# Kernel tuning notes

Measured on AMD Instinct MI355X. Metric: run time of the kernel, lower is better.

Reference implementation:

```python
import jax, jax.numpy as jnp
import numpy as np

R, K, CF, HF, WF = 64, 81, 256, 256, 256  # ROIs, classes(incl bg), FPN channels, P2 size
IMG = 1024.0
SCALE = 0.25          # P2 feature stride 4
STEPS = 4             # subdivision steps: 7 -> 112
NPTS = 28 * 28        # subdivision_num_points
FC = 256


def _grid_sample(img, coords):
    """torch.grid_sample(bilinear, align_corners=False, zeros padding).
    img: [N,C,H,W]; coords: [N,P,2] (x,y) in [0,1]. Returns [N,C,P]."""
    N, C, H, W = img.shape
    x = coords[..., 0] * W - 0.5
    y = coords[..., 1] * H - 0.5
    x0 = jnp.floor(x); y0 = jnp.floor(y)
    fx = x - x0; fy = y - y0

    def g(ix, iy, w):
        valid = (ix >= 0) & (ix < W) & (iy >= 0) & (iy < H)
        ixc = jnp.clip(ix, 0, W - 1).astype(jnp.int32)
        iyc = jnp.clip(iy, 0, H - 1).astype(jnp.int32)
        v = jax.vmap(lambda im, yy, xx: im[:, yy, xx])(img, iyc, ixc)  # [N,C,P]
        return v * (w * valid)[:, None, :]

    return (g(x0, y0, (1 - fx) * (1 - fy)) + g(x0 + 1, y0, fx * (1 - fy))
            + g(x0, y0 + 1, (1 - fx) * fy) + g(x0 + 1, y0 + 1, fx * fy))


def _point_head(fine, coarse, W1, b1, W2, b2, W3, b3, Wp, bp):
    # StandardPointHead: 1x1-conv fc layers, coarse logits re-concatenated each layer
    x = jnp.concatenate([fine, coarse], axis=1)  # [R, CF+K, P]
    for Wl, bl in ((W1, b1), (W2, b2), (W3, b3)):
        x = jax.nn.relu(jnp.einsum('oc,rcp->rop', Wl, x) + bl[None, :, None])
        x = jnp.concatenate([x, coarse], axis=1)
    return jnp.einsum('oc,rcp->rop', Wp, x) + bp[None, :, None]  # [R,K,P]


def setup_inputs() -> dict:
    key = jax.random.key(0)
    ks = jax.random.split(key, 12)
    feat = jax.random.normal(ks[0], (1, CF, HF, WF), dtype=jnp.float32)
    u = jax.random.uniform(ks[1], (R, 4), dtype=jnp.float32)
    x0 = u[:, 0] * (IMG - 256.0); y0 = u[:, 1] * (IMG - 256.0)
    w = 32.0 + u[:, 2] * 224.0;   h = 32.0 + u[:, 3] * 224.0
    det_bboxes = jnp.stack([x0, y0, x0 + w, y0 + h], axis=1)
    det_labels = jax.random.randint(ks[2], (R,), 0, 80, dtype=jnp.int32)
    coarse_logits = jax.random.normal(ks[3], (R, K, 7, 7), dtype=jnp.float32)
    cin = CF + K  # = FC + K = 337 for all layers here
    s = 0.02
    return {
        'feat': feat, 'det_bboxes': det_bboxes, 'det_labels': det_labels,
        'coarse_logits': coarse_logits,
        'W1': jax.random.normal(ks[4], (FC, cin), jnp.float32) * s,
        'b1': jnp.zeros((FC,), jnp.float32),
        'W2': jax.random.normal(ks[5], (FC, FC + K), jnp.float32) * s,
        'b2': jnp.zeros((FC,), jnp.float32),
        'W3': jax.random.normal(ks[6], (FC, FC + K), jnp.float32) * s,
        'b3': jnp.zeros((FC,), jnp.float32),
        'Wp': jax.random.normal(ks[7], (K, FC + K), jnp.float32) * s,
        'bp': jnp.zeros((K,), jnp.float32),
    }


def reference(feat, det_bboxes, det_labels, coarse_logits,
              W1, b1, W2, b2, W3, b3, Wp, bp):
    ml = coarse_logits
    bx0, by0 = det_bboxes[:, 0], det_bboxes[:, 1]
    bw = det_bboxes[:, 2] - det_bboxes[:, 0]
    bh = det_bboxes[:, 3] - det_bboxes[:, 1]
    for step in range(STEPS):
        _, _, H, W = ml.shape
        H, W = 2 * H, 2 * W
        # bilinear x2, align_corners=False (half-pixel centers)
        ml = jax.image.resize(ml, (R, K, H, W), method='linear')
        if NPTS >= 4 * H * W and step < STEPS - 1:
            continue
        # uncertainty = -|logit of gt class| (det_labels+1 skips background ch 0)
        gt = ml[jnp.arange(R), det_labels + 1]              # [R,H,W]
        unc = -jnp.abs(gt).reshape(R, H * W)
        _, idx = jax.lax.top_k(unc, NPTS)                   # [R,NPTS]
        px = ((idx % W).astype(ml.dtype) + 0.5) / W
        py = ((idx // W).astype(ml.dtype) + 0.5) / H
        coords = jnp.stack([px, py], axis=-1)               # [R,NPTS,2] in ROI [0,1]
        # project ROI coords to image, then to P2 normalized coords
        cx = bx0[:, None] + coords[..., 0] * bw[:, None]
        cy = by0[:, None] + coords[..., 1] * bh[:, None]
        fcoords = jnp.stack([cx * SCALE / WF, cy * SCALE / HF], axis=-1)
        fine = _grid_sample(feat, fcoords.reshape(1, R * NPTS, 2))  # [1,CF,R*NPTS]
        fine = fine[0].reshape(CF, R, NPTS).transpose(1, 0, 2)      # [R,CF,NPTS]
        coarse = _grid_sample(coarse_logits, coords)                # [R,K,NPTS]
        pl = _point_head(fine, coarse, W1, b1, W2, b2, W3, b3, Wp, bp)
        ml = jax.vmap(lambda m, i, p: m.at[:, i].set(p))(
            ml.reshape(R, K, H * W), idx, pl).reshape(R, K, H, W)
    return ml
```

## Files before the change

### kernel.cpp

```cpp
#include <hip/hip_runtime.h>
#include <hip/hip_bf16.h>
#include <cstdint>
#include <cstddef>

#define R_ 64
#define K_ 81
#define NPTS_ 784

typedef __attribute__((ext_vector_type(8))) short short8;
typedef __attribute__((ext_vector_type(4))) float f32x4;

#define GLDS16(G, L)                                                           \
  __builtin_amdgcn_global_load_lds(                                            \
      (__attribute__((address_space(1))) void*)(void*)(G),                     \
      (__attribute__((address_space(3))) void*)(L), 16, 0, 0)

__global__ __launch_bounds__(256) void transpose_feat_kernel(const float* __restrict__ in,
                                                             float* __restrict__ out) {
  __shared__ float tile[32][33];
  int y = blockIdx.z;
  int x0 = blockIdx.x * 32, c0 = blockIdx.y * 32;
  int tx = threadIdx.x, ty = threadIdx.y;
#pragma unroll
  for (int j = 0; j < 32; j += 8)
    tile[ty + j][tx] = in[(size_t)(c0 + ty + j) * 65536 + (size_t)y * 256 + x0 + tx];
  __syncthreads();
#pragma unroll
  for (int j = 0; j < 32; j += 8)
    out[((size_t)y * 256 + (x0 + ty + j)) * 256 + c0 + tx] = tile[tx][ty + j];
}

__global__ void transpose_coarse_kernel(const float* __restrict__ in, float* __restrict__ out) {
  int t = blockIdx.x * 256 + threadIdx.x;
  if (t >= R_ * 49 * K_) return;
  int k = t % K_;
  int t2 = t / K_;
  int pos = t2 % 49;
  int r = t2 / 49;
  out[t] = in[((size_t)r * K_ + k) * 49 + pos];
}

__global__ void prep_wpack_kernel(const float* __restrict__ W1, const float* __restrict__ W2,
                                  const float* __restrict__ W3, const float* __restrict__ Wp,
                                  const float* __restrict__ b1, const float* __restrict__ b2,
                                  const float* __restrict__ b3, const float* __restrict__ bp,
                                  __hip_bfloat16* __restrict__ Wpk, float* __restrict__ bias_all) {
  int t = blockIdx.x * 256 + threadIdx.x;
  if (t < 90112) {
    int lane = t & 63;
    int t2 = t >> 6;
    int hl = t2 & 1;
    t2 >>= 1;
    int jg = t2 & 15;
    t2 >>= 4;
    int kt = t2 % 11;
    int L = t2 / 11;
    int o = jg * 16 + (lane & 15);
    int kbase = kt * 32 + (lane >> 4) * 8;
    const float* Wsrc = (L == 0) ? W1 : (L == 1) ? W2 : (L == 2) ? W3 : Wp;
    int Omax = (L == 3) ? 81 : 256;
    __hip_bfloat16 outv[8];
#pragma unroll
    for (int e = 0; e < 8; ++e) {
      int k = kbase + e;
      float v = (o < Omax && k < 337) ? Wsrc[o * 337 + k] : 0.f;
      __hip_bfloat16 h = __float2bfloat16(v);
      outv[e] = hl ? __float2bfloat16(v - __bfloat162float(h)) : h;
    }
    *(short8*)(Wpk + (size_t)t * 8) = *(const short8*)outv;
  } else if (t < 90112 + 1024) {
    int k = t - 90112;
    float v = 0.f;
    if (k < 256) v = b1[k];
    else if (k < 512) v = b2[k - 256];
    else if (k < 768) v = b3[k - 512];
    else if (k < 768 + 81) v = bp[k - 768];
    bias_all[k] = v;
  }
}

__global__ __launch_bounds__(128) void upsample2x_kernel(const float* __restrict__ in,
                                                         float* __restrict__ out,
                                                         int Hin, int Win) {
  int b = blockIdx.z;
  int iy = blockIdx.y * 2 + threadIdx.y;
  int ix = blockIdx.x * 64 + threadIdx.x;
  if (ix >= Win || iy >= Hin) return;
  const float* p = in + (size_t)b * Hin * Win;
  int rT = (iy == 0) ? 0 : iy - 1;
  int rB = (iy == Hin - 1) ? iy : iy + 1;
  int cL = (ix == 0) ? 0 : ix - 1;
  int cR = (ix == Win - 1) ? ix : ix + 1;
  float wyT1 = (iy == 0) ? 0.f : 0.75f;
  float wyB1 = (iy == Hin - 1) ? 0.f : 0.25f;
  float wxE1 = (ix == 0) ? 0.f : 0.75f;
  float wxO1 = (ix == Win - 1) ? 0.f : 0.25f;
  float wyT0 = 1.f - wyT1, wyB0 = 1.f - wyB1;
  float wxE0 = 1.f - wxE1, wxO0 = 1.f - wxO1;

  const float* rowA = p + (size_t)rT * Win;
  const float* rowM = p + (size_t)iy * Win;
  const float* rowC = p + (size_t)rB * Win;
  float al = rowA[cL], am = rowA[ix], ar = rowA[cR];
  float mL = rowM[cL], mm = rowM[ix], mr = rowM[cR];
  float cl = rowC[cL], cm = rowC[ix], cr = rowC[cR];

  float aE = wxE0 * al + wxE1 * am;
  float aO = wxO0 * am + wxO1 * ar;
  float mE = wxE0 * mL + wxE1 * mm;
  float mO = wxO0 * mm + wxO1 * mr;
  float cE = wxE0 * cl + wxE1 * cm;
  float cO = wxO0 * cm + wxO1 * cr;

  float oTE = wyT0 * aE + wyT1 * mE;
  float oTO = wyT0 * aO + wyT1 * mO;
  float oBE = wyB0 * mE + wyB1 * cE;
  float oBO = wyB0 * mO + wyB1 * cO;

  int Wout = 2 * Win;
  float* ob = out + ((size_t)b * (2 * Hin) + 2 * iy) * Wout + 2 * ix;
  *(float2*)ob = make_float2(oTE, oTO);
  *(float2*)(ob + Wout) = make_float2(oBE, oBO);
}

__global__ void iota_kernel(int* __restrict__ sel) {
  int t = blockIdx.x * 256 + threadIdx.x;
  if (t < R_ * NPTS_) sel[t] = t % NPTS_;
}

__global__ __launch_bounds__(256) void topk_kernel(const float* __restrict__ ml,
                                                   const int* __restrict__ labels,
                                                   int N, int* __restrict__ sel) {
  int r = blockIdx.x;
  const float* gt = ml + ((size_t)r * K_ + (labels[r] + 1)) * N;
  __shared__ unsigned int hist[256];
  __shared__ unsigned int sh_prefix, sh_remaining, sh_countless;
  int tid = threadIdx.x;

  unsigned int prefix = 0;
  unsigned int remaining = NPTS_;
  unsigned int count_less = 0;
  for (int pass = 0; pass < 4; ++pass) {
    int shift = 24 - 8 * pass;
    hist[tid] = 0;
    __syncthreads();
    for (int i = tid; i < N; i += 256) {
      unsigned int v = __float_as_uint(fabsf(gt[i]));
      bool match = (pass == 0) || ((v >> (shift + 8)) == prefix);
      if (match) atomicAdd(&hist[(v >> shift) & 255u], 1u);
    }
    __syncthreads();
    if (tid == 0) {
      unsigned int cum = 0, before = 0;
      int d = 255;
      for (int dd = 0; dd < 256; ++dd) {
        unsigned int c = hist[dd];
        if (cum + c >= remaining) { before = cum; d = dd; break; }
        cum += c;
      }
      sh_prefix = (prefix << 8) | (unsigned int)d;
      sh_remaining = remaining - before;
      sh_countless = count_less + before;
    }
    __syncthreads();
    prefix = sh_prefix;
    remaining = sh_remaining;
    count_less = sh_countless;
    __syncthreads();
  }
  unsigned int vstar = prefix;
  unsigned int need_eq = NPTS_ - count_less;

  __shared__ unsigned int wtot_less[4], wtot_eq[4];
  unsigned int base_less = 0, base_eq = 0;
  int lane = tid & 63, wv = tid >> 6;
  int* selr = sel + (size_t)r * NPTS_;
  for (int base = 0; base < N; base += 256) {
    int i = base + tid;
    bool less = false, eq = false;
    if (i < N) {
      unsigned int v = __float_as_uint(fabsf(gt[i]));
      less = v < vstar;
      eq = v == vstar;
    }
    unsigned long long ml_ = __ballot(less);
    unsigned long long me_ = __ballot(eq);
    unsigned long long lanemask = (lane == 0) ? 0ull : ((~0ull) >> (64 - lane));
    unsigned int pl = __popcll(ml_ & lanemask);
    unsigned int pe = __popcll(me_ & lanemask);
    if (lane == 0) { wtot_less[wv] = (unsigned int)__popcll(ml_); wtot_eq[wv] = (unsigned int)__popcll(me_); }
    __syncthreads();
    unsigned int off_l = 0, off_e = 0, tot_l = 0, tot_e = 0;
#pragma unroll
    for (int w2 = 0; w2 < 4; ++w2) {
      unsigned int tl = wtot_less[w2], te = wtot_eq[w2];
      if (w2 < wv) { off_l += tl; off_e += te; }
      tot_l += tl;
      tot_e += te;
    }
    if (less) selr[base_less + off_l + pl] = i;
    if (eq) {
      unsigned int er = base_eq + off_e + pe;
      if (er < need_eq) selr[count_less + er] = i;
    }
    base_less += tot_l;
    base_eq += tot_e;
    __syncthreads();
  }
}

__global__ __launch_bounds__(256) void sample_kernel(const int* __restrict__ sel,
                                                     const float* __restrict__ bboxes,
                                                     const float* __restrict__ featT,
                                                     const float* __restrict__ coarseT,
                                                     __hip_bfloat16* __restrict__ Xh,
                                                     __hip_bfloat16* __restrict__ Xl,
                                                     __hip_bfloat16* __restrict__ Cth,
                                                     __hip_bfloat16* __restrict__ Ctl,
                                                     int Wlev, int Hlev) {
  int rp = blockIdx.x;
  int r = rp / NPTS_;
  int idx = sel[rp];
  int tid = threadIdx.x;

  float px = ((float)(idx % Wlev) + 0.5f) / (float)Wlev;
  float py = ((float)(idx / Wlev) + 0.5f) / (float)Hlev;
  float bx0 = bboxes[r * 4 + 0], by0 = bboxes[r * 4 + 1];
  float bw = __fsub_rn(bboxes[r * 4 + 2], bx0);
  float bh = __fsub_rn(bboxes[r * 4 + 3], by0);
  float cx = __fadd_rn(bx0, __fmul_rn(px, bw));
  float cy = __fadd_rn(by0, __fmul_rn(py, bh));

  {
    float gx = __fsub_rn(__fmul_rn(cx, 0.25f), 0.5f);
    float gy = __fsub_rn(__fmul_rn(cy, 0.25f), 0.5f);
    float fxf = floorf(gx), fyf = floorf(gy);
    float fx = __fsub_rn(gx, fxf), fy = __fsub_rn(gy, fyf);
    int x0 = (int)fxf, y0 = (int)fyf;
    float ofx = __fsub_rn(1.f, fx), ofy = __fsub_rn(1.f, fy);
    float w00 = __fmul_rn(ofx, ofy);
    float w10 = __fmul_rn(fx, ofy);
    float w01 = __fmul_rn(ofx, fy);
    float w11 = __fmul_rn(fx, fy);
    bool vx0 = (x0 >= 0) && (x0 < 256), vx1 = (x0 + 1 >= 0) && (x0 + 1 < 256);
    bool vy0 = (y0 >= 0) && (y0 < 256), vy1 = (y0 + 1 >= 0) && (y0 + 1 < 256);
    float W00 = (vx0 && vy0) ? w00 : 0.f;
    float W10 = (vx1 && vy0) ? w10 : 0.f;
    float W01 = (vx0 && vy1) ? w01 : 0.f;
    float W11 = (vx1 && vy1) ? w11 : 0.f;
    int x0c = min(max(x0, 0), 255), x1c = min(max(x0 + 1, 0), 255);
    int y0c = min(max(y0, 0), 255), y1c = min(max(y0 + 1, 0), 255);
    const float* p00 = featT + ((size_t)(y0c * 256 + x0c)) * 256;
    const float* p10 = featT + ((size_t)(y0c * 256 + x1c)) * 256;
    const float* p01 = featT + ((size_t)(y1c * 256 + x0c)) * 256;
    const float* p11 = featT + ((size_t)(y1c * 256 + x1c)) * 256;
    float acc = __fmul_rn(p00[tid], W00);
    acc = __fadd_rn(acc, __fmul_rn(p10[tid], W10));
    acc = __fadd_rn(acc, __fmul_rn(p01[tid], W01));
    acc = __fadd_rn(acc, __fmul_rn(p11[tid], W11));
    __hip_bfloat16 h = __float2bfloat16(acc);
    Xh[(size_t)rp * 256 + tid] = h;
    Xl[(size_t)rp * 256 + tid] = __float2bfloat16(acc - __bfloat162float(h));
  }

  if (tid < 96) {
    float acc = 0.f;
    if (tid < K_) {
      float gx = __fsub_rn(__fmul_rn(px, 7.f), 0.5f);
      float gy = __fsub_rn(__fmul_rn(py, 7.f), 0.5f);
      float fxf = floorf(gx), fyf = floorf(gy);
      float fx = __fsub_rn(gx, fxf), fy = __fsub_rn(gy, fyf);
      int x0 = (int)fxf, y0 = (int)fyf;
      float ofx = __fsub_rn(1.f, fx), ofy = __fsub_rn(1.f, fy);
      float w00 = __fmul_rn(ofx, ofy);
      float w10 = __fmul_rn(fx, ofy);
      float w01 = __fmul_rn(ofx, fy);
      float w11 = __fmul_rn(fx, fy);
      bool vx0 = (x0 >= 0) && (x0 < 7), vx1 = (x0 + 1 >= 0) && (x0 + 1 < 7);
      bool vy0 = (y0 >= 0) && (y0 < 7), vy1 = (y0 + 1 >= 0) && (y0 + 1 < 7);
      float W00 = (vx0 && vy0) ? w00 : 0.f;
      float W10 = (vx1 && vy0) ? w10 : 0.f;
      float W01 = (vx0 && vy1) ? w01 : 0.f;
      float W11 = (vx1 && vy1) ? w11 : 0.f;
      int x0c = min(max(x0, 0), 6), x1c = min(max(x0 + 1, 0), 6);
      int y0c = min(max(y0, 0), 6), y1c = min(max(y0 + 1, 0), 6);
      const float* cb = coarseT + (size_t)r * 49 * K_;
      acc = __fmul_rn(cb[(size_t)(y0c * 7 + x0c) * K_ + tid], W00);
      acc = __fadd_rn(acc, __fmul_rn(cb[(size_t)(y0c * 7 + x1c) * K_ + tid], W10));
      acc = __fadd_rn(acc, __fmul_rn(cb[(size_t)(y1c * 7 + x0c) * K_ + tid], W01));
      acc = __fadd_rn(acc, __fmul_rn(cb[(size_t)(y1c * 7 + x1c) * K_ + tid], W11));
    }
    __hip_bfloat16 h = __float2bfloat16(acc);
    Cth[(size_t)rp * 96 + tid] = h;
    Ctl[(size_t)rp * 96 + tid] = __float2bfloat16(acc - __bfloat162float(h));
  }
}

template <int TERMS>
__global__ __launch_bounds__(256, 2) void fused_head_kernel(
    const __hip_bfloat16* __restrict__ Ah, const __hip_bfloat16* __restrict__ Al,
    const __hip_bfloat16* __restrict__ Th, const __hip_bfloat16* __restrict__ Tl,
    const __hip_bfloat16* __restrict__ Wpk,
    const float* __restrict__ bias_all, float* __restrict__ PL) {
  constexpr int XPLANE = 11 * 4096;
  constexpr int XLO = 8 * 4096;
  __shared__ char lds[(TERMS == 3) ? XPLANE + XLO : XPLANE];
  char* Xh = lds;
  char* Xl = lds + XPLANE;

  const int tid = threadIdx.x;
  const int lane = tid & 63;
  const int w = tid >> 6;
  const int g = lane >> 4;
  const int lane15 = lane & 15;
  const int m0 = blockIdx.x * 64;

  {
    const int srow = tid >> 2;
    const int sp = tid & 3;
    const int sx = sp ^ ((srow >> 1) & 3);
#pragma unroll
    for (int kt = 0; kt < 8; ++kt) {
      size_t off = (((size_t)(m0 + srow)) * 256 + (size_t)kt * 32 + (size_t)sx * 8) * 2;
      GLDS16((const char*)Ah + off, Xh + kt * 4096 + w * 1024);
      if constexpr (TERMS == 3) GLDS16((const char*)Al + off, Xl + kt * 4096 + w * 1024);
    }
#pragma unroll
    for (int kt = 8; kt < 11; ++kt) {
      size_t off = (((size_t)(m0 + srow)) * 96 + (size_t)(kt - 8) * 32 + (size_t)sx * 8) * 2;
      GLDS16((const char*)Th + off, Xh + kt * 4096 + w * 1024);
    }
  }
  asm volatile("s_waitcnt vmcnt(0)" ::: "memory");
  __syncthreads();

  int offA[4];
#pragma unroll
  for (int i = 0; i < 4; ++i) {
    int rowA = i * 16 + lane15;
    offA[i] = rowA * 64 + ((g ^ ((rowA >> 1) & 3)) << 4);
  }

#pragma unroll 1
  for (int L = 0; L < 4; ++L) {
    if (L == 3 && w >= 2) break;
    const __hip_bfloat16* WL = Wpk + (size_t)L * (11 * 16 * 2 * 512);

    f32x4 acc[4][4];
#pragma unroll
    for (int i = 0; i < 4; ++i)
#pragma unroll
      for (int j = 0; j < 4; ++j) acc[i][j] = (f32x4){0.f, 0.f, 0.f, 0.f};

    short8 a_h[2][4], a_l[2][4], b_h[2][4], b_l[2][4];
#pragma unroll
    for (int i = 0; i < 4; ++i) {
      a_h[0][i] = *(const short8*)(Xh + offA[i]);
      if constexpr (TERMS == 3) a_l[0][i] = *(const short8*)(Xl + offA[i]);
    }
#pragma unroll
    for (int j = 0; j < 4; ++j) {
      const __hip_bfloat16* bp = WL + (((size_t)0 * 16 + (w * 4 + j)) * 2) * 512 + (size_t)lane * 8;
      b_h[0][j] = *(const short8*)bp;
      if constexpr (TERMS == 3) b_l[0][j] = *(const short8*)(bp + 512);
    }

#pragma unroll
    for (int kt = 0; kt < 11; ++kt) {
      const int c = kt & 1, n = c ^ 1;
      if (kt < 10) {
        const int ktn = kt + 1;
#pragma unroll
        for (int i = 0; i < 4; ++i) {
          a_h[n][i] = *(const short8*)(Xh + ktn * 4096 + offA[i]);
          if constexpr (TERMS == 3) {
            if (ktn < 8)
              a_l[n][i] = *(const short8*)(Xl + ktn * 4096 + offA[i]);
            else
              a_l[n][i] = *(const short8*)((const char*)Tl +
                  (((size_t)(m0 + i * 16 + lane15)) * 96 + (size_t)(ktn - 8) * 32 +
                   (size_t)g * 8) * 2);
          }
        }
#pragma unroll
        for (int j = 0; j < 4; ++j) {
          const __hip_bfloat16* bp =
              WL + (((size_t)ktn * 16 + (w * 4 + j)) * 2) * 512 + (size_t)lane * 8;
          b_h[n][j] = *(const short8*)bp;
          if constexpr (TERMS == 3) b_l[n][j] = *(const short8*)(bp + 512);
        }
      }
#pragma unroll
      for (int i = 0; i < 4; ++i)
#pragma unroll
        for (int j = 0; j < 4; ++j) {
          acc[i][j] = __builtin_amdgcn_mfma_f32_16x16x32_bf16(a_h[c][i], b_h[c][j], acc[i][j], 0, 0, 0);
          if constexpr (TERMS == 3) {
            acc[i][j] = __builtin_amdgcn_mfma_f32_16x16x32_bf16(a_h[c][i], b_l[c][j], acc[i][j], 0, 0, 0);
            acc[i][j] = __builtin_amdgcn_mfma_f32_16x16x32_bf16(a_l[c][i], b_h[c][j], acc[i][j], 0, 0, 0);
          }
        }
    }

    if (L < 3) {
      __syncthreads();
#pragma unroll
      for (int j = 0; j < 4; ++j) {
        int o = w * 64 + j * 16 + lane15;
        float bv = bias_all[L * 256 + o];
        int kch = o >> 5;
        int s0 = (o >> 3) & 3;
        int e = o & 7;
#pragma unroll
        for (int i = 0; i < 4; ++i) {
          int mb = i * 16 + g * 4;
#pragma unroll
          for (int r = 0; r < 4; ++r) {
            int m = mb + r;
            float v = fmaxf(acc[i][j][r] + bv, 0.f);
            __hip_bfloat16 h = __float2bfloat16(v);
            int boff = kch * 4096 + m * 64 + ((s0 ^ ((m >> 1) & 3)) << 4) + e * 2;
            *(__hip_bfloat16*)(Xh + boff) = h;
            if constexpr (TERMS == 3)
              *(__hip_bfloat16*)(Xl + boff) = __float2bfloat16(v - __bfloat162float(h));
          }
        }
      }
      __syncthreads();
    } else {
#pragma unroll
      for (int j = 0; j < 4; ++j) {
        int o = w * 64 + j * 16 + lane15;
        float bv = bias_all[768 + o];
#pragma unroll
        for (int i = 0; i < 4; ++i) {
          int mb = i * 16 + g * 4;
#pragma unroll
          for (int r = 0; r < 4; ++r)
            PL[(size_t)(m0 + mb + r) * 128 + o] = acc[i][j][r] + bv;
        }
      }
    }
  }
}

__global__ void scatter_kernel(const float* __restrict__ PL, const int* __restrict__ sel,
                               float* __restrict__ ml, int Nlev) {
  int t = blockIdx.x * 256 + threadIdx.x;
  if (t >= R_ * NPTS_ * K_) return;
  int k = t % K_;
  int rp = t / K_;
  int i = sel[rp];
  int r = rp / NPTS_;
  ml[((size_t)r * K_ + k) * Nlev + i] = PL[(size_t)rp * 128 + k];
}

extern "C" void kernel_launch(void* const* d_in, const int* in_sizes, int n_in,
                              void* d_out, int out_size, void* d_ws, size_t ws_size,
                              hipStream_t stream) {
  (void)in_sizes; (void)n_in; (void)out_size; (void)ws_size;
  const float* feat = (const float*)d_in[0];
  const float* bboxes = (const float*)d_in[1];
  const int* labels = (const int*)d_in[2];
  const float* coarse = (const float*)d_in[3];
  const float* W1 = (const float*)d_in[4];
  const float* b1 = (const float*)d_in[5];
  const float* W2 = (const float*)d_in[6];
  const float* b2 = (const float*)d_in[7];
  const float* W3 = (const float*)d_in[8];
  const float* b3 = (const float*)d_in[9];
  const float* Wp = (const float*)d_in[10];
  const float* bp = (const float*)d_in[11];
  float* out = (float*)d_out;

  char* p = (char*)d_ws;
  auto alloc = [&](size_t bytes) { char* r = p; p += (bytes + 255) & ~(size_t)255; return r; };
  float* featT = (float*)alloc(16777216ull * 4);
  float* coarseT = (float*)alloc(254016ull * 4);
  float* ml14 = (float*)alloc(1016064ull * 4);
  float* ml28 = (float*)alloc(4064256ull * 4);
  float* ml56 = (float*)alloc(16257024ull * 4);
  float* PL = (float*)alloc(6422528ull * 4);
  int* sel = (int*)alloc(50176ull * 4);
  __hip_bfloat16* Xa_h = (__hip_bfloat16*)alloc(12845056ull * 2);
  __hip_bfloat16* Xa_l = (__hip_bfloat16*)alloc(12845056ull * 2);
  __hip_bfloat16* Ct_h = (__hip_bfloat16*)alloc(4816896ull * 2);
  __hip_bfloat16* Ct_l = (__hip_bfloat16*)alloc(4816896ull * 2);
  __hip_bfloat16* Wpk = (__hip_bfloat16*)alloc(720896ull * 2);
  float* bias_all = (float*)alloc(1024ull * 4);

  const int N = R_ * NPTS_;
  const int B = R_ * K_;

  transpose_feat_kernel<<<dim3(8, 8, 256), dim3(32, 8), 0, stream>>>(feat, featT);
  transpose_coarse_kernel<<<3969, 256, 0, stream>>>(coarse, coarseT);
  prep_wpack_kernel<<<357, 256, 0, stream>>>(W1, W2, W3, Wp, b1, b2, b3, bp, Wpk, bias_all);

  upsample2x_kernel<<<dim3(1, 4, B), dim3(64, 2), 0, stream>>>(coarse, ml14, 7, 7);

  upsample2x_kernel<<<dim3(1, 7, B), dim3(64, 2), 0, stream>>>(ml14, ml28, 14, 14);
  iota_kernel<<<196, 256, 0, stream>>>(sel);
  sample_kernel<<<N, 256, 0, stream>>>(sel, bboxes, featT, coarseT, Xa_h, Xa_l, Ct_h, Ct_l, 28, 28);
  fused_head_kernel<3><<<784, 256, 0, stream>>>(Xa_h, Xa_l, Ct_h, Ct_l, Wpk, bias_all, PL);
  scatter_kernel<<<15876, 256, 0, stream>>>(PL, sel, ml28, 784);

  upsample2x_kernel<<<dim3(1, 14, B), dim3(64, 2), 0, stream>>>(ml28, ml56, 28, 28);
  topk_kernel<<<R_, 256, 0, stream>>>(ml56, labels, 3136, sel);
  sample_kernel<<<N, 256, 0, stream>>>(sel, bboxes, featT, coarseT, Xa_h, Xa_l, Ct_h, Ct_l, 56, 56);
  fused_head_kernel<3><<<784, 256, 0, stream>>>(Xa_h, Xa_l, Ct_h, Ct_l, Wpk, bias_all, PL);
  scatter_kernel<<<15876, 256, 0, stream>>>(PL, sel, ml56, 3136);

  upsample2x_kernel<<<dim3(1, 28, B), dim3(64, 2), 0, stream>>>(ml56, out, 56, 56);
  topk_kernel<<<R_, 256, 0, stream>>>(out, labels, 12544, sel);
  sample_kernel<<<N, 256, 0, stream>>>(sel, bboxes, featT, coarseT, Xa_h, Xa_l, Ct_h, Ct_l, 112, 112);
  fused_head_kernel<1><<<784, 256, 0, stream>>>(Xa_h, nullptr, Ct_h, nullptr, Wpk, bias_all, PL);
  scatter_kernel<<<15876, 256, 0, stream>>>(PL, sel, out, 12544);
}
```

Before: 919.2 us.

## Fuse feature bilinear sampling and result scatter into the point-head kernel

The fine-feature grid sampling moves into the fused MLP head kernel, which now gathers featT rows straight into swizzled LDS tiles (hi/lo bf16 split), so the Xa_h/Xa_l global intermediates go away. The final layer writes its logits directly into the mask-logit map, which removes the PL buffer and the separate scatter kernel. Coarse sampling becomes its own 96-thread kernel. The B-operand prefetch depth becomes templated (deeper for the single-term path) and s_setprio is placed around the MFMA blocks. The cost is a serial gather phase inside the GEMM kernel before any MFMA work starts, and scattered, uncoalesced output stores.

Result: slower. 959.5 us (+4.4%).

```diff
diff --git a/kernel.cpp b/kernel.cpp
--- a/kernel.cpp
+++ b/kernel.cpp
@@ -209,15 +209,12 @@
   }
 }
 
-__global__ __launch_bounds__(256) void sample_kernel(const int* __restrict__ sel,
-                                                     const float* __restrict__ bboxes,
-                                                     const float* __restrict__ featT,
-                                                     const float* __restrict__ coarseT,
-                                                     __hip_bfloat16* __restrict__ Xh,
-                                                     __hip_bfloat16* __restrict__ Xl,
-                                                     __hip_bfloat16* __restrict__ Cth,
-                                                     __hip_bfloat16* __restrict__ Ctl,
-                                                     int Wlev, int Hlev) {
+__global__ __launch_bounds__(96) void coarse_sample_kernel(const int* __restrict__ sel,
+                                                           const float* __restrict__ bboxes,
+                                                           const float* __restrict__ coarseT,
+                                                           __hip_bfloat16* __restrict__ Cth,
+                                                           __hip_bfloat16* __restrict__ Ctl,
+                                                           int Wlev, int Hlev) {
   int rp = blockIdx.x;
   int r = rp / NPTS_;
   int idx = sel[rp];
@@ -225,13 +222,85 @@
 
   float px = ((float)(idx % Wlev) + 0.5f) / (float)Wlev;
   float py = ((float)(idx / Wlev) + 0.5f) / (float)Hlev;
-  float bx0 = bboxes[r * 4 + 0], by0 = bboxes[r * 4 + 1];
-  float bw = __fsub_rn(bboxes[r * 4 + 2], bx0);
-  float bh = __fsub_rn(bboxes[r * 4 + 3], by0);
-  float cx = __fadd_rn(bx0, __fmul_rn(px, bw));
-  float cy = __fadd_rn(by0, __fmul_rn(py, bh));
+
+  float acc = 0.f;
+  if (tid < K_) {
+    float gx = __fsub_rn(__fmul_rn(px, 7.f), 0.5f);
+    float gy = __fsub_rn(__fmul_rn(py, 7.f), 0.5f);
+    float fxf = floorf(gx), fyf = floorf(gy);
+    float fx = __fsub_rn(gx, fxf), fy = __fsub_rn(gy, fyf);
+    int x0 = (int)fxf, y0 = (int)fyf;
+    float ofx = __fsub_rn(1.f, fx), ofy = __fsub_rn(1.f, fy);
+    float w00 = __fmul_rn(ofx, ofy);
+    float w10 = __fmul_rn(fx, ofy);
+    float w01 = __fmul_rn(ofx, fy);
+    float w11 = __fmul_rn(fx, fy);
+    bool vx0 = (x0 >= 0) && (x0 < 7), vx1 = (x0 + 1 >= 0) && (x0 + 1 < 7);
+    bool vy0 = (y0 >= 0) && (y0 < 7), vy1 = (y0 + 1 >= 0) && (y0 + 1 < 7);
+    float W00 = (vx0 && vy0) ? w00 : 0.f;
+    float W10 = (vx1 && vy0) ? w10 : 0.f;
+    float W01 = (vx0 && vy1) ? w01 : 0.f;
+    float W11 = (vx1 && vy1) ? w11 : 0.f;
+    int x0c = min(max(x0, 0), 6), x1c = min(max(x0 + 1, 0), 6);
+    int y0c = min(max(y0, 0), 6), y1c = min(max(y0 + 1, 0), 6);
+    const float* cb = coarseT + (size_t)r * 49 * K_;
+    acc = __fmul_rn(cb[(size_t)(y0c * 7 + x0c) * K_ + tid], W00);
+    acc = __fadd_rn(acc, __fmul_rn(cb[(size_t)(y0c * 7 + x1c) * K_ + tid], W10));
+    acc = __fadd_rn(acc, __fmul_rn(cb[(size_t)(y1c * 7 + x0c) * K_ + tid], W01));
+    acc = __fadd_rn(acc, __fmul_rn(cb[(size_t)(y1c * 7 + x1c) * K_ + tid], W11));
+  }
+  __hip_bfloat16 h = __float2bfloat16(acc);
+  Cth[(size_t)rp * 96 + tid] = h;
+  Ctl[(size_t)rp * 96 + tid] = __float2bfloat16(acc - __bfloat162float(h));
+}
+
+template <int TERMS>
+__global__ __launch_bounds__(256, 2) void fused_head_kernel(
+    const int* __restrict__ sel, const float* __restrict__ bboxes,
+    const float* __restrict__ featT,
+    const __hip_bfloat16* __restrict__ Th, const __hip_bfloat16* __restrict__ Tl,
+    const __hip_bfloat16* __restrict__ Wpk,
+    const float* __restrict__ bias_all, float* __restrict__ ml,
+    int Wlev, int Hlev) {
+  constexpr int XPLANE = 11 * 4096;
+  constexpr int XLO = 8 * 4096;
+  constexpr int XSZ = (TERMS == 3) ? XPLANE + XLO : XPLANE;
+  __shared__ char lds[XSZ + 2048];
+  char* Xh = lds;
+  char* Xl = lds + XPLANE;
+  float* sW = (float*)(lds + XSZ);
+  int* sO = (int*)(lds + XSZ + 1024);
+
+  const int tid = threadIdx.x;
+  const int lane = tid & 63;
+  const int w = tid >> 6;
+  const int g = lane >> 4;
+  const int lane15 = lane & 15;
+  const int m0 = blockIdx.x * 64;
+  const int Nlev = Wlev * Hlev;
 
   {
+    const int srow = tid >> 2;
+    const int sp = tid & 3;
+    const int sx = sp ^ ((srow >> 1) & 3);
+#pragma unroll
+    for (int kt = 8; kt < 11; ++kt) {
+      size_t off = (((size_t)(m0 + srow)) * 96 + (size_t)(kt - 8) * 32 + (size_t)sx * 8) * 2;
+      GLDS16((const char*)Th + off, Xh + kt * 4096 + w * 1024);
+    }
+  }
+
+  if (tid < 64) {
+    int m = m0 + tid;
+    int idx = sel[m];
+    int r = m / NPTS_;
+    float px = ((float)(idx % Wlev) + 0.5f) / (float)Wlev;
+    float py = ((float)(idx / Wlev) + 0.5f) / (float)Hlev;
+    float bx0 = bboxes[r * 4 + 0], by0 = bboxes[r * 4 + 1];
+    float bw = __fsub_rn(bboxes[r * 4 + 2], bx0);
+    float bh = __fsub_rn(bboxes[r * 4 + 3], by0);
+    float cx = __fadd_rn(bx0, __fmul_rn(px, bw));
+    float cy = __fadd_rn(by0, __fmul_rn(py, bh));
     float gx = __fsub_rn(__fmul_rn(cx, 0.25f), 0.5f);
     float gy = __fsub_rn(__fmul_rn(cy, 0.25f), 0.5f);
     float fxf = floorf(gx), fyf = floorf(gy);
@@ -244,94 +313,39 @@
     float w11 = __fmul_rn(fx, fy);
     bool vx0 = (x0 >= 0) && (x0 < 256), vx1 = (x0 + 1 >= 0) && (x0 + 1 < 256);
     bool vy0 = (y0 >= 0) && (y0 < 256), vy1 = (y0 + 1 >= 0) && (y0 + 1 < 256);
-    float W00 = (vx0 && vy0) ? w00 : 0.f;
-    float W10 = (vx1 && vy0) ? w10 : 0.f;
-    float W01 = (vx0 && vy1) ? w01 : 0.f;
-    float W11 = (vx1 && vy1) ? w11 : 0.f;
+    sW[tid * 4 + 0] = (vx0 && vy0) ? w00 : 0.f;
+    sW[tid * 4 + 1] = (vx1 && vy0) ? w10 : 0.f;
+    sW[tid * 4 + 2] = (vx0 && vy1) ? w01 : 0.f;
+    sW[tid * 4 + 3] = (vx1 && vy1) ? w11 : 0.f;
     int x0c = min(max(x0, 0), 255), x1c = min(max(x0 + 1, 0), 255);
     int y0c = min(max(y0, 0), 255), y1c = min(max(y0 + 1, 0), 255);
-    const float* p00 = featT + ((size_t)(y0c * 256 + x0c)) * 256;
-    const float* p10 = featT + ((size_t)(y0c * 256 + x1c)) * 256;
-    const float* p01 = featT + ((size_t)(y1c * 256 + x0c)) * 256;
-    const float* p11 = featT + ((size_t)(y1c * 256 + x1c)) * 256;
-    float acc = __fmul_rn(p00[tid], W00);
-    acc = __fadd_rn(acc, __fmul_rn(p10[tid], W10));
-    acc = __fadd_rn(acc, __fmul_rn(p01[tid], W01));
-    acc = __fadd_rn(acc, __fmul_rn(p11[tid], W11));
-    __hip_bfloat16 h = __float2bfloat16(acc);
-    Xh[(size_t)rp * 256 + tid] = h;
-    Xl[(size_t)rp * 256 + tid] = __float2bfloat16(acc - __bfloat162float(h));
-  }
-
-  if (tid < 96) {
-    float acc = 0.f;
-    if (tid < K_) {
-      float gx = __fsub_rn(__fmul_rn(px, 7.f), 0.5f);
-      float gy = __fsub_rn(__fmul_rn(py, 7.f), 0.5f);
-      float fxf = floorf(gx), fyf = floorf(gy);
-      float fx = __fsub_rn(gx, fxf), fy = __fsub_rn(gy, fyf);
-      int x0 = (int)fxf, y0 = (int)fyf;
-      float ofx = __fsub_rn(1.f, fx), ofy = __fsub_rn(1.f, fy);
-      float w00 = __fmul_rn(ofx, ofy);
-      float w10 = __fmul_rn(fx, ofy);
-      float w01 = __fmul_rn(ofx, fy);
-      float w11 = __fmul_rn(fx, fy);
-      bool vx0 = (x0 >= 0) && (x0 < 7), vx1 = (x0 + 1 >= 0) && (x0 + 1 < 7);
-      bool vy0 = (y0 >= 0) && (y0 < 7), vy1 = (y0 + 1 >= 0) && (y0 + 1 < 7);
-      float W00 = (vx0 && vy0) ? w00 : 0.f;
-      float W10 = (vx1 && vy0) ? w10 : 0.f;
-      float W01 = (vx0 && vy1) ? w01 : 0.f;
-      float W11 = (vx1 && vy1) ? w11 : 0.f;
-      int x0c = min(max(x0, 0), 6), x1c = min(max(x0 + 1, 0), 6);
-      int y0c = min(max(y0, 0), 6), y1c = min(max(y0 + 1, 0), 6);
-      const float* cb = coarseT + (size_t)r * 49 * K_;
-      acc = __fmul_rn(cb[(size_t)(y0c * 7 + x0c) * K_ + tid], W00);
-      acc = __fadd_rn(acc, __fmul_rn(cb[(size_t)(y0c * 7 + x1c) * K_ + tid], W10));
-      acc = __fadd_rn(acc, __fmul_rn(cb[(size_t)(y1c * 7 + x0c) * K_ + tid], W01));
-      acc = __fadd_rn(acc, __fmul_rn(cb[(size_t)(y1c * 7 + x1c) * K_ + tid], W11));
-    }
-    __hip_bfloat16 h = __float2bfloat16(acc);
-    Cth[(size_t)rp * 96 + tid] = h;
-    Ctl[(size_t)rp * 96 + tid] = __float2bfloat16(acc - __bfloat162float(h));
-  }
-}
-
-template <int TERMS>
-__global__ __launch_bounds__(256, 2) void fused_head_kernel(
-    const __hip_bfloat16* __restrict__ Ah, const __hip_bfloat16* __restrict__ Al,
-    const __hip_bfloat16* __restrict__ Th, const __hip_bfloat16* __restrict__ Tl,
-    const __hip_bfloat16* __restrict__ Wpk,
-    const float* __restrict__ bias_all, float* __restrict__ PL) {
-  constexpr int XPLANE = 11 * 4096;
-  constexpr int XLO = 8 * 4096;
-  __shared__ char lds[(TERMS == 3) ? XPLANE + XLO : XPLANE];
-  char* Xh = lds;
-  char* Xl = lds + XPLANE;
-
-  const int tid = threadIdx.x;
-  const int lane = tid & 63;
-  const int w = tid >> 6;
-  const int g = lane >> 4;
-  const int lane15 = lane & 15;
-  const int m0 = blockIdx.x * 64;
+    sO[tid * 4 + 0] = (y0c * 256 + x0c) * 256;
+    sO[tid * 4 + 1] = (y0c * 256 + x1c) * 256;
+    sO[tid * 4 + 2] = (y1c * 256 + x0c) * 256;
+    sO[tid * 4 + 3] = (y1c * 256 + x1c) * 256;
+  }
+  __syncthreads();
 
   {
-    const int srow = tid >> 2;
-    const int sp = tid & 3;
-    const int sx = sp ^ ((srow >> 1) & 3);
-#pragma unroll
-    for (int kt = 0; kt < 8; ++kt) {
-      size_t off = (((size_t)(m0 + srow)) * 256 + (size_t)kt * 32 + (size_t)sx * 8) * 2;
-      GLDS16((const char*)Ah + off, Xh + kt * 4096 + w * 1024);
-      if constexpr (TERMS == 3) GLDS16((const char*)Al + off, Xl + kt * 4096 + w * 1024);
-    }
-#pragma unroll
-    for (int kt = 8; kt < 11; ++kt) {
-      size_t off = (((size_t)(m0 + srow)) * 96 + (size_t)(kt - 8) * 32 + (size_t)sx * 8) * 2;
-      GLDS16((const char*)Th + off, Xh + kt * 4096 + w * 1024);
-    }
-  }
-  asm volatile("s_waitcnt vmcnt(0)" ::: "memory");
+    const int ch = tid;
+    const int kch = ch >> 5;
+    const int s0c = (ch >> 3) & 3;
+    const int e = ch & 7;
+#pragma unroll 4
+    for (int mm = 0; mm < 64; ++mm) {
+      float4 wv = *(const float4*)(sW + mm * 4);
+      int4 ov = *(const int4*)(sO + mm * 4);
+      float acc = __fmul_rn(featT[(size_t)ov.x + ch], wv.x);
+      acc = __fadd_rn(acc, __fmul_rn(featT[(size_t)ov.y + ch], wv.y));
+      acc = __fadd_rn(acc, __fmul_rn(featT[(size_t)ov.z + ch], wv.z));
+      acc = __fadd_rn(acc, __fmul_rn(featT[(size_t)ov.w + ch], wv.w));
+      __hip_bfloat16 h = __float2bfloat16(acc);
+      int boff = kch * 4096 + mm * 64 + ((s0c ^ ((mm >> 1) & 3)) << 4) + e * 2;
+      *(__hip_bfloat16*)(Xh + boff) = h;
+      if constexpr (TERMS == 3)
+        *(__hip_bfloat16*)(Xl + boff) = __float2bfloat16(acc - __bfloat162float(h));
+    }
+  }
   __syncthreads();
 
   int offA[4];
@@ -340,6 +354,8 @@
     int rowA = i * 16 + lane15;
     offA[i] = rowA * 64 + ((g ^ ((rowA >> 1) & 3)) << 4);
   }
+
+  constexpr int BD = (TERMS == 1) ? 3 : 2;
 
 #pragma unroll 1
   for (int L = 0; L < 4; ++L) {
@@ -352,54 +368,54 @@
 #pragma unroll
       for (int j = 0; j < 4; ++j) acc[i][j] = (f32x4){0.f, 0.f, 0.f, 0.f};
 
-    short8 a_h[2][4], a_l[2][4], b_h[2][4], b_l[2][4];
-#pragma unroll
-    for (int i = 0; i < 4; ++i) {
-      a_h[0][i] = *(const short8*)(Xh + offA[i]);
-      if constexpr (TERMS == 3) a_l[0][i] = *(const short8*)(Xl + offA[i]);
-    }
-#pragma unroll
-    for (int j = 0; j < 4; ++j) {
-      const __hip_bfloat16* bp = WL + (((size_t)0 * 16 + (w * 4 + j)) * 2) * 512 + (size_t)lane * 8;
-      b_h[0][j] = *(const short8*)bp;
-      if constexpr (TERMS == 3) b_l[0][j] = *(const short8*)(bp + 512);
-    }
+    short8 a_h[2][4], a_l[2][4], b_h[BD][4], b_l[BD][4];
+
+    auto loadA = [&](int buf, int kt) {
+#pragma unroll
+      for (int i = 0; i < 4; ++i) {
+        a_h[buf][i] = *(const short8*)(Xh + kt * 4096 + offA[i]);
+        if constexpr (TERMS == 3) {
+          if (kt < 8)
+            a_l[buf][i] = *(const short8*)(Xl + kt * 4096 + offA[i]);
+          else
+            a_l[buf][i] = *(const short8*)((const char*)Tl +
+                (((size_t)(m0 + i * 16 + lane15)) * 96 + (size_t)(kt - 8) * 32 +
+                 (size_t)g * 8) * 2);
+        }
+      }
+    };
+    auto loadB = [&](int buf, int kt) {
+#pragma unroll
+      for (int j = 0; j < 4; ++j) {
+        const __hip_bfloat16* bp =
+            WL + (((size_t)kt * 16 + (w * 4 + j)) * 2) * 512 + (size_t)lane * 8;
+        b_h[buf][j] = *(const short8*)bp;
+        if constexpr (TERMS == 3) b_l[buf][j] = *(const short8*)(bp + 512);
+      }
+    };
+
+    loadA(0, 0);
+#pragma unroll
+    for (int pb = 0; pb < BD - 1; ++pb) loadB(pb, pb);
 
 #pragma unroll
     for (int kt = 0; kt < 11; ++kt) {
-      const int c = kt & 1, n = c ^ 1;
-      if (kt < 10) {
-        const int ktn = kt + 1;
-#pragma unroll
-        for (int i = 0; i < 4; ++i) {
-          a_h[n][i] = *(const short8*)(Xh + ktn * 4096 + offA[i]);
+      const int ca = kt & 1;
+      const int cb = kt % BD;
+      if (kt < 10) loadA(ca ^ 1, kt + 1);
+      if (kt + BD - 1 < 11) loadB((kt + BD - 1) % BD, kt + BD - 1);
+      __builtin_amdgcn_s_setprio(1);
+#pragma unroll
+      for (int i = 0; i < 4; ++i)
+#pragma unroll
+        for (int j = 0; j < 4; ++j) {
+          acc[i][j] = __builtin_amdgcn_mfma_f32_16x16x32_bf16(a_h[ca][i], b_h[cb][j], acc[i][j], 0, 0, 0);
           if constexpr (TERMS == 3) {
-            if (ktn < 8)
-              a_l[n][i] = *(const short8*)(Xl + ktn * 4096 + offA[i]);
-            else
-              a_l[n][i] = *(const short8*)((const char*)Tl +
-                  (((size_t)(m0 + i * 16 + lane15)) * 96 + (size_t)(ktn - 8) * 32 +
-                   (size_t)g * 8) * 2);
+            acc[i][j] = __builtin_amdgcn_mfma_f32_16x16x32_bf16(a_h[ca][i], b_l[cb][j], acc[i][j], 0, 0, 0);
+            acc[i][j] = __builtin_amdgcn_mfma_f32_16x16x32_bf16(a_l[ca][i], b_h[cb][j], acc[i][j], 0, 0, 0);
           }
         }
-#pragma unroll
-        for (int j = 0; j < 4; ++j) {
-          const __hip_bfloat16* bp =
-              WL + (((size_t)ktn * 16 + (w * 4 + j)) * 2) * 512 + (size_t)lane * 8;
-          b_h[n][j] = *(const short8*)bp;
-          if constexpr (TERMS == 3) b_l[n][j] = *(const short8*)(bp + 512);
-        }
-      }
-#pragma unroll
-      for (int i = 0; i < 4; ++i)
-#pragma unroll
-        for (int j = 0; j < 4; ++j) {
-          acc[i][j] = __builtin_amdgcn_mfma_f32_16x16x32_bf16(a_h[c][i], b_h[c][j], acc[i][j], 0, 0, 0);
-          if constexpr (TERMS == 3) {
-            acc[i][j] = __builtin_amdgcn_mfma_f32_16x16x32_bf16(a_h[c][i], b_l[c][j], acc[i][j], 0, 0, 0);
-            acc[i][j] = __builtin_amdgcn_mfma_f32_16x16x32_bf16(a_l[c][i], b_h[c][j], acc[i][j], 0, 0, 0);
-          }
-        }
+      __builtin_amdgcn_s_setprio(0);
     }
 
     if (L < 3) {
@@ -431,28 +447,23 @@
 #pragma unroll
       for (int j = 0; j < 4; ++j) {
         int o = w * 64 + j * 16 + lane15;
-        float bv = bias_all[768 + o];
-#pragma unroll
-        for (int i = 0; i < 4; ++i) {
-          int mb = i * 16 + g * 4;
-#pragma unroll
-          for (int r = 0; r < 4; ++r)
-            PL[(size_t)(m0 + mb + r) * 128 + o] = acc[i][j][r] + bv;
+        if (o < K_) {
+          float bv = bias_all[768 + o];
+#pragma unroll
+          for (int i = 0; i < 4; ++i) {
+            int mb = i * 16 + g * 4;
+#pragma unroll
+            for (int r = 0; r < 4; ++r) {
+              int m = m0 + mb + r;
+              int idx = sel[m];
+              int rroi = m / NPTS_;
+              ml[((size_t)rroi * K_ + o) * Nlev + idx] = acc[i][j][r] + bv;
+            }
+          }
         }
       }
     }
   }
-}
-
-__global__ void scatter_kernel(const float* __restrict__ PL, const int* __restrict__ sel,
-                               float* __restrict__ ml, int Nlev) {
-  int t = blockIdx.x * 256 + threadIdx.x;
-  if (t >= R_ * NPTS_ * K_) return;
-  int k = t % K_;
-  int rp = t / K_;
-  int i = sel[rp];
-  int r = rp / NPTS_;
-  ml[((size_t)r * K_ + k) * Nlev + i] = PL[(size_t)rp * 128 + k];
 }
 
 extern "C" void kernel_launch(void* const* d_in, const int* in_sizes, int n_in,
@@ -480,10 +491,7 @@
   float* ml14 = (float*)alloc(1016064ull * 4);
   float* ml28 = (float*)alloc(4064256ull * 4);
   float* ml56 = (float*)alloc(16257024ull * 4);
-  float* PL = (float*)alloc(6422528ull * 4);
   int* sel = (int*)alloc(50176ull * 4);
-  __hip_bfloat16* Xa_h = (__hip_bfloat16*)alloc(12845056ull * 2);
-  __hip_bfloat16* Xa_l = (__hip_bfloat16*)alloc(12845056ull * 2);
   __hip_bfloat16* Ct_h = (__hip_bfloat16*)alloc(4816896ull * 2);
   __hip_bfloat16* Ct_l = (__hip_bfloat16*)alloc(4816896ull * 2);
   __hip_bfloat16* Wpk = (__hip_bfloat16*)alloc(720896ull * 2);
@@ -500,19 +508,16 @@
 
   upsample2x_kernel<<<dim3(1, 7, B), dim3(64, 2), 0, stream>>>(ml14, ml28, 14, 14);
   iota_kernel<<<196, 256, 0, stream>>>(sel);
-  sample_kernel<<<N, 256, 0, stream>>>(sel, bboxes, featT, coarseT, Xa_h, Xa_l, Ct_h, Ct_l, 28, 28);
-  fused_head_kernel<3><<<784, 256, 0, stream>>>(Xa_h, Xa_l, Ct_h, Ct_l, Wpk, bias_all, PL);
-  scatter_kernel<<<15876, 256, 0, stream>>>(PL, sel, ml28, 784);
+  coarse_sample_kernel<<<N, 96, 0, stream>>>(sel, bboxes, coarseT, Ct_h, Ct_l, 28, 28);
+  fused_head_kernel<3><<<784, 256, 0, stream>>>(sel, bboxes, featT, Ct_h, Ct_l, Wpk, bias_all, ml28, 28, 28);
 
   upsample2x_kernel<<<dim3(1, 14, B), dim3(64, 2), 0, stream>>>(ml28, ml56, 28, 28);
   topk_kernel<<<R_, 256, 0, stream>>>(ml56, labels, 3136, sel);
-  sample_kernel<<<N, 256, 0, stream>>>(sel, bboxes, featT, coarseT, Xa_h, Xa_l, Ct_h, Ct_l, 56, 56);
-  fused_head_kernel<3><<<784, 256, 0, stream>>>(Xa_h, Xa_l, Ct_h, Ct_l, Wpk, bias_all, PL);
-  scatter_kernel<<<15876, 256, 0, stream>>>(PL, sel, ml56, 3136);
+  coarse_sample_kernel<<<N, 96, 0, stream>>>(sel, bboxes, coarseT, Ct_h, Ct_l, 56, 56);
+  fused_head_kernel<3><<<784, 256, 0, stream>>>(sel, bboxes, featT, Ct_h, Ct_l, Wpk, bias_all, ml56, 56, 56);
 
   upsample2x_kernel<<<dim3(1, 28, B), dim3(64, 2), 0, stream>>>(ml56, out, 56, 56);
   topk_kernel<<<R_, 256, 0, stream>>>(out, labels, 12544, sel);
-  sample_kernel<<<N, 256, 0, stream>>>(sel, bboxes, featT, coarseT, Xa_h, Xa_l, Ct_h, Ct_l, 112, 112);
-  fused_head_kernel<1><<<784, 256, 0, stream>>>(Xa_h, nullptr, Ct_h, nullptr, Wpk, bias_all, PL);
-  scatter_kernel<<<15876, 256, 0, stream>>>(PL, sel, out, 12544);
-}
+  coarse_sample_kernel<<<N, 96, 0, stream>>>(sel, bboxes, coarseT, Ct_h, Ct_l, 112, 112);
+  fused_head_kernel<1><<<784, 256, 0, stream>>>(sel, bboxes, featT, Ct_h, nullptr, Wpk, bias_all, out, 112, 112);
+}
```

## Fuse scatter into point-head kernel and deepen weight prefetch pipeline

Applied to the files above, without the earlier changes.

The separate scatter kernel and the PL staging buffer are removed. The final-layer epilogue of the fused head kernel now writes logits straight into the mask at the selected indices, with a guard for o<81. The K-loop is also restructured: B operands use a 3-deep prefetch buffer in the single-term variant, and s_setprio raises wave priority around the MFMA block. This saves three launches and a global round trip of PL. In exchange the scatter stores are strided and uncoalesced, and register pressure rises.

After: 966.4 us. +5.1%, slower.

```diff
diff --git a/kernel.cpp b/kernel.cpp
--- a/kernel.cpp
+++ b/kernel.cpp
@@ -301,7 +301,8 @@
     const __hip_bfloat16* __restrict__ Ah, const __hip_bfloat16* __restrict__ Al,
     const __hip_bfloat16* __restrict__ Th, const __hip_bfloat16* __restrict__ Tl,
     const __hip_bfloat16* __restrict__ Wpk,
-    const float* __restrict__ bias_all, float* __restrict__ PL) {
+    const float* __restrict__ bias_all,
+    const int* __restrict__ sel, float* __restrict__ ml, int Nlev) {
   constexpr int XPLANE = 11 * 4096;
   constexpr int XLO = 8 * 4096;
   __shared__ char lds[(TERMS == 3) ? XPLANE + XLO : XPLANE];
@@ -341,6 +342,8 @@
     offA[i] = rowA * 64 + ((g ^ ((rowA >> 1) & 3)) << 4);
   }
 
+  constexpr int BD = (TERMS == 1) ? 3 : 2;
+
 #pragma unroll 1
   for (int L = 0; L < 4; ++L) {
     if (L == 3 && w >= 2) break;
@@ -352,54 +355,54 @@
 #pragma unroll
       for (int j = 0; j < 4; ++j) acc[i][j] = (f32x4){0.f, 0.f, 0.f, 0.f};
 
-    short8 a_h[2][4], a_l[2][4], b_h[2][4], b_l[2][4];
-#pragma unroll
-    for (int i = 0; i < 4; ++i) {
-      a_h[0][i] = *(const short8*)(Xh + offA[i]);
-      if constexpr (TERMS == 3) a_l[0][i] = *(const short8*)(Xl + offA[i]);
-    }
-#pragma unroll
-    for (int j = 0; j < 4; ++j) {
-      const __hip_bfloat16* bp = WL + (((size_t)0 * 16 + (w * 4 + j)) * 2) * 512 + (size_t)lane * 8;
-      b_h[0][j] = *(const short8*)bp;
-      if constexpr (TERMS == 3) b_l[0][j] = *(const short8*)(bp + 512);
-    }
+    short8 a_h[2][4], a_l[2][4], b_h[BD][4], b_l[BD][4];
+
+    auto loadA = [&](int buf, int kt) {
+#pragma unroll
+      for (int i = 0; i < 4; ++i) {
+        a_h[buf][i] = *(const short8*)(Xh + kt * 4096 + offA[i]);
+        if constexpr (TERMS == 3) {
+          if (kt < 8)
+            a_l[buf][i] = *(const short8*)(Xl + kt * 4096 + offA[i]);
+          else
+            a_l[buf][i] = *(const short8*)((const char*)Tl +
+                (((size_t)(m0 + i * 16 + lane15)) * 96 + (size_t)(kt - 8) * 32 +
+                 (size_t)g * 8) * 2);
+        }
+      }
+    };
+    auto loadB = [&](int buf, int kt) {
+#pragma unroll
+      for (int j = 0; j < 4; ++j) {
+        const __hip_bfloat16* bp =
+            WL + (((size_t)kt * 16 + (w * 4 + j)) * 2) * 512 + (size_t)lane * 8;
+        b_h[buf][j] = *(const short8*)bp;
+        if constexpr (TERMS == 3) b_l[buf][j] = *(const short8*)(bp + 512);
+      }
+    };
+
+    loadA(0, 0);
+#pragma unroll
+    for (int pb = 0; pb < BD - 1; ++pb) loadB(pb, pb);
 
 #pragma unroll
     for (int kt = 0; kt < 11; ++kt) {
-      const int c = kt & 1, n = c ^ 1;
-      if (kt < 10) {
-        const int ktn = kt + 1;
-#pragma unroll
-        for (int i = 0; i < 4; ++i) {
-          a_h[n][i] = *(const short8*)(Xh + ktn * 4096 + offA[i]);
+      const int ca = kt & 1;
+      const int cb = kt % BD;
+      if (kt < 10) loadA(ca ^ 1, kt + 1);
+      if (kt + BD - 1 < 11) loadB((kt + BD - 1) % BD, kt + BD - 1);
+      __builtin_amdgcn_s_setprio(1);
+#pragma unroll
+      for (int i = 0; i < 4; ++i)
+#pragma unroll
+        for (int j = 0; j < 4; ++j) {
+          acc[i][j] = __builtin_amdgcn_mfma_f32_16x16x32_bf16(a_h[ca][i], b_h[cb][j], acc[i][j], 0, 0, 0);
           if constexpr (TERMS == 3) {
-            if (ktn < 8)
-              a_l[n][i] = *(const short8*)(Xl + ktn * 4096 + offA[i]);
-            else
-              a_l[n][i] = *(const short8*)((const char*)Tl +
-                  (((size_t)(m0 + i * 16 + lane15)) * 96 + (size_t)(ktn - 8) * 32 +
-                   (size_t)g * 8) * 2);
+            acc[i][j] = __builtin_amdgcn_mfma_f32_16x16x32_bf16(a_h[ca][i], b_l[cb][j], acc[i][j], 0, 0, 0);
+            acc[i][j] = __builtin_amdgcn_mfma_f32_16x16x32_bf16(a_l[ca][i], b_h[cb][j], acc[i][j], 0, 0, 0);
           }
         }
-#pragma unroll
-        for (int j = 0; j < 4; ++j) {
-          const __hip_bfloat16* bp =
-              WL + (((size_t)ktn * 16 + (w * 4 + j)) * 2) * 512 + (size_t)lane * 8;
-          b_h[n][j] = *(const short8*)bp;
-          if constexpr (TERMS == 3) b_l[n][j] = *(const short8*)(bp + 512);
-        }
-      }
-#pragma unroll
-      for (int i = 0; i < 4; ++i)
-#pragma unroll
-        for (int j = 0; j < 4; ++j) {
-          acc[i][j] = __builtin_amdgcn_mfma_f32_16x16x32_bf16(a_h[c][i], b_h[c][j], acc[i][j], 0, 0, 0);
-          if constexpr (TERMS == 3) {
-            acc[i][j] = __builtin_amdgcn_mfma_f32_16x16x32_bf16(a_h[c][i], b_l[c][j], acc[i][j], 0, 0, 0);
-            acc[i][j] = __builtin_amdgcn_mfma_f32_16x16x32_bf16(a_l[c][i], b_h[c][j], acc[i][j], 0, 0, 0);
-          }
-        }
+      __builtin_amdgcn_s_setprio(0);
     }
 
     if (L < 3) {
@@ -431,28 +434,23 @@
 #pragma unroll
       for (int j = 0; j < 4; ++j) {
         int o = w * 64 + j * 16 + lane15;
-        float bv = bias_all[768 + o];
-#pragma unroll
-        for (int i = 0; i < 4; ++i) {
-          int mb = i * 16 + g * 4;
-#pragma unroll
-          for (int r = 0; r < 4; ++r)
-            PL[(size_t)(m0 + mb + r) * 128 + o] = acc[i][j][r] + bv;
+        if (o < K_) {
+          float bv = bias_all[768 + o];
+#pragma unroll
+          for (int i = 0; i < 4; ++i) {
+            int mb = i * 16 + g * 4;
+#pragma unroll
+            for (int r = 0; r < 4; ++r) {
+              int m = m0 + mb + r;
+              int idx = sel[m];
+              int rroi = m / NPTS_;
+              ml[((size_t)rroi * K_ + o) * Nlev + idx] = acc[i][j][r] + bv;
+            }
+          }
         }
       }
     }
   }
-}
-
-__global__ void scatter_kernel(const float* __restrict__ PL, const int* __restrict__ sel,
-                               float* __restrict__ ml, int Nlev) {
-  int t = blockIdx.x * 256 + threadIdx.x;
-  if (t >= R_ * NPTS_ * K_) return;
-  int k = t % K_;
-  int rp = t / K_;
-  int i = sel[rp];
-  int r = rp / NPTS_;
-  ml[((size_t)r * K_ + k) * Nlev + i] = PL[(size_t)rp * 128 + k];
 }
 
 extern "C" void kernel_launch(void* const* d_in, const int* in_sizes, int n_in,
@@ -480,7 +478,6 @@
   float* ml14 = (float*)alloc(1016064ull * 4);
   float* ml28 = (float*)alloc(4064256ull * 4);
   float* ml56 = (float*)alloc(16257024ull * 4);
-  float* PL = (float*)alloc(6422528ull * 4);
   int* sel = (int*)alloc(50176ull * 4);
   __hip_bfloat16* Xa_h = (__hip_bfloat16*)alloc(12845056ull * 2);
   __hip_bfloat16* Xa_l = (__hip_bfloat16*)alloc(12845056ull * 2);
@@ -501,18 +498,15 @@
   upsample2x_kernel<<<dim3(1, 7, B), dim3(64, 2), 0, stream>>>(ml14, ml28, 14, 14);
   iota_kernel<<<196, 256, 0, stream>>>(sel);
   sample_kernel<<<N, 256, 0, stream>>>(sel, bboxes, featT, coarseT, Xa_h, Xa_l, Ct_h, Ct_l, 28, 28);
-  fused_head_kernel<3><<<784, 256, 0, stream>>>(Xa_h, Xa_l, Ct_h, Ct_l, Wpk, bias_all, PL);
-  scatter_kernel<<<15876, 256, 0, stream>>>(PL, sel, ml28, 784);
+  fused_head_kernel<3><<<784, 256, 0, stream>>>(Xa_h, Xa_l, Ct_h, Ct_l, Wpk, bias_all, sel, ml28, 784);
 
   upsample2x_kernel<<<dim3(1, 14, B), dim3(64, 2), 0, stream>>>(ml28, ml56, 28, 28);
   topk_kernel<<<R_, 256, 0, stream>>>(ml56, labels, 3136, sel);
   sample_kernel<<<N, 256, 0, stream>>>(sel, bboxes, featT, coarseT, Xa_h, Xa_l, Ct_h, Ct_l, 56, 56);
-  fused_head_kernel<3><<<784, 256, 0, stream>>>(Xa_h, Xa_l, Ct_h, Ct_l, Wpk, bias_all, PL);
-  scatter_kernel<<<15876, 256, 0, stream>>>(PL, sel, ml56, 3136);
+  fused_head_kernel<3><<<784, 256, 0, stream>>>(Xa_h, Xa_l, Ct_h, Ct_l, Wpk, bias_all, sel, ml56, 3136);
 
   upsample2x_kernel<<<dim3(1, 28, B), dim3(64, 2), 0, stream>>>(ml56, out, 56, 56);
   topk_kernel<<<R_, 256, 0, stream>>>(out, labels, 12544, sel);
   sample_kernel<<<N, 256, 0, stream>>>(sel, bboxes, featT, coarseT, Xa_h, Xa_l, Ct_h, Ct_l, 112, 112);
-  fused_head_kernel<1><<<784, 256, 0, stream>>>(Xa_h, nullptr, Ct_h, nullptr, Wpk, bias_all, PL);
-  scatter_kernel<<<15876, 256, 0, stream>>>(PL, sel, out, 12544);
-}
+  fused_head_kernel<1><<<784, 256, 0, stream>>>(Xa_h, nullptr, Ct_h, nullptr, Wpk, bias_all, sel, out, 12544);
+}
```
